# Kernel optimization log

Measured on AMD Instinct MI355X. Metric: run time of the kernel, lower is better.

Reference implementation:

```python
import jax, jax.numpy as jnp
import numpy as np

N, DEG, F = 500000, 16, 128
H1, H2, OUT = 256, 256, 128


def setup_inputs() -> dict:
    key = jax.random.key(0)
    ks = jax.random.split(key, 8)
    s = lambda fan_in: 1.0 / np.sqrt(fan_in)
    return {
        "message": jax.random.normal(ks[0], (N, DEG, F), dtype=jnp.float32),
        "features": jax.random.normal(ks[1], (N, F), dtype=jnp.float32),
        "global_features": jax.random.normal(ks[2], (N, F), dtype=jnp.float32),
        "W1": jax.random.normal(ks[3], (3 * F, H1), dtype=jnp.float32) * s(3 * F),
        "b1": jnp.zeros((H1,), dtype=jnp.float32),
        "W2": jax.random.normal(ks[4], (H1, H2), dtype=jnp.float32) * s(H1),
        "b2": jnp.zeros((H2,), dtype=jnp.float32),
        "W3": jax.random.normal(ks[5], (H2, OUT), dtype=jnp.float32) * s(H2),
        "b3": jnp.zeros((OUT,), dtype=jnp.float32),
    }


def reference(message, features, global_features, W1, b1, W2, b2, W3, b3):
    # mailbox sum-aggregate over neighbors: [N, deg, F] -> [N, F]
    agg = jnp.sum(message, axis=1)
    # concat aggregated messages with node + global features: [N, 3F]
    x = jnp.concatenate([agg, features, global_features], axis=1)
    # MLP: Linear+ReLU, Linear+ReLU, Linear
    h = jax.nn.relu(x @ W1 + b1)
    h = jax.nn.relu(h @ W2 + b2)
    out = h @ W3 + b3
    # row-wise L2 (Frobenius over dim=1) normalization
    norm = jnp.linalg.norm(out, axis=1, keepdims=True)
    return out / (norm + 1e-8)
```

## Files before the change

kernel.cpp:

```cpp
#include <hip/hip_runtime.h>


typedef short short8   __attribute__((ext_vector_type(8)));
typedef short short4_t __attribute__((ext_vector_type(4)));
typedef float f32x4    __attribute__((ext_vector_type(4)));

#define SWZ(row, off) ((off) ^ (((row) & 7) << 4))

__device__ __forceinline__ unsigned short f2bf(float f) {
    unsigned int u = __float_as_uint(f);
    u += 0x7fffu + ((u >> 16) & 1u);
    return (unsigned short)(u >> 16);
}

__global__ void prep_weights(const float* __restrict__ W1,
                             const float* __restrict__ W2,
                             const float* __restrict__ W3,
                             short* __restrict__ pw1,
                             short* __restrict__ pw2,
                             short* __restrict__ pw3) {
    int idx = blockIdx.x * 256 + threadIdx.x;
    if (idx < 98304) {
        int j = idx & 7, l = (idx >> 3) & 63, g = idx >> 9;
        int ks = g % 12, tn = g / 12;
        int n = tn * 16 + (l & 15);
        int k = ks * 32 + ((l >> 4) << 3) + j;
        pw1[idx] = (short)f2bf(W1[k * 256 + n]);
    } else if (idx < 98304 + 65536) {
        int e = idx - 98304;
        int j = e & 7, l = (e >> 3) & 63, g = e >> 9;
        int ks = g & 7, tn = g >> 3;
        int n = tn * 16 + (l & 15);
        int k = ks * 32 + ((l >> 4) << 3) + j;
        pw2[e] = (short)f2bf(W2[k * 256 + n]);
    } else if (idx < 98304 + 65536 + 32768) {
        int e = idx - 98304 - 65536;
        int j = e & 7, l = (e >> 3) & 63, g = e >> 9;
        int ks = g & 7, tn = g >> 3;
        int n = tn * 16 + (l & 15);
        int k = ks * 32 + ((l >> 4) << 3) + j;
        pw3[e] = (short)f2bf(W3[k * 128 + n]);
    }
}

__global__ __launch_bounds__(256) void agg_kernel(
    const float* __restrict__ msg, short* __restrict__ agg, int n_rows)
{
    const int w = threadIdx.x >> 6;
    const int l = threadIdx.x & 63;
    const long long pb = (long long)blockIdx.x * 8 + 2 * w;
    if (pb >= n_rows) return;

    const f32x4* base = (const f32x4*)((const char*)msg + pb * 8192);
    f32x4 tA[8], tB[8];
    const bool okB = (pb + 1) < n_rows;
    #pragma unroll
    for (int i = 0; i < 8; ++i) tA[i] = __builtin_nontemporal_load(base + i * 64 + l);
    if (okB) {
        #pragma unroll
        for (int i = 0; i < 8; ++i) tB[i] = __builtin_nontemporal_load(base + (8 + i) * 64 + l);
    } else {
        #pragma unroll
        for (int i = 0; i < 8; ++i) tB[i] = (f32x4){0.f, 0.f, 0.f, 0.f};
    }
    f32x4 sA = ((tA[0] + tA[1]) + (tA[2] + tA[3])) + ((tA[4] + tA[5]) + (tA[6] + tA[7]));
    f32x4 sB = ((tB[0] + tB[1]) + (tB[2] + tB[3])) + ((tB[4] + tB[5]) + (tB[6] + tB[7]));
    #pragma unroll
    for (int c = 0; c < 4; ++c) {
        sA[c] += __shfl_xor(sA[c], 32);
        sB[c] += __shfl_xor(sB[c], 32);
    }
    f32x4 s = (l < 32) ? sA : sB;
    short4_t s4;
    s4[0] = (short)f2bf(s[0]); s4[1] = (short)f2bf(s[1]);
    s4[2] = (short)f2bf(s[2]); s4[3] = (short)f2bf(s[3]);
    const long long orow = pb + (l >> 5);
    if (orow < n_rows)
        *(short4_t*)(agg + orow * 128 + (l & 31) * 4) = s4;
}

__global__ __launch_bounds__(256, 4) void node_net(
    const short* __restrict__ aggb,
    const float* __restrict__ feat,
    const float* __restrict__ glob,
    const float* __restrict__ b1v,
    const float* __restrict__ b2v,
    const float* __restrict__ b3v,
    const short* __restrict__ pw1,
    const short* __restrict__ pw2,
    const short* __restrict__ pw3,
    float* __restrict__ out,
    int n_rows)
{
    __shared__ char lds[32768];
    char* regA = lds;
    char* regB = lds + 16384;

    const int tid  = threadIdx.x;
    const int lane = tid & 63;
    const int w    = tid >> 6;
    const int lr   = lane & 15;
    const int lk   = lane >> 4;
    const long long r0 = (long long)blockIdx.x * 32;

    const f32x4 zero4 = {0.f, 0.f, 0.f, 0.f};

    f32x4 fr[4], gr[4];
    #pragma unroll
    for (int q = 0; q < 4; ++q) {
        int r = (tid >> 5) + q * 8;
        long long row = r0 + r;
        fr[q] = zero4; gr[q] = zero4;
        if (row < n_rows) {
            fr[q] = __builtin_nontemporal_load((const f32x4*)feat + row * 32 + (tid & 31));
            gr[q] = __builtin_nontemporal_load((const f32x4*)glob + row * 32 + (tid & 31));
        }
    }

    #pragma unroll
    for (int pass = 0; pass < 2; ++pass) {
        int r = tid >> 3;
        int c = (tid & 7) + 8 * pass;
        long long row = r0 + r;
        short8 v = {0, 0, 0, 0, 0, 0, 0, 0};
        if (row < n_rows) v = __builtin_nontemporal_load((const short8*)(aggb + row * 128 + c * 8));
        *(short8*)(regB + SWZ(r, r * 256 + c * 16)) = v;
    }
    __syncthreads();

    #pragma unroll
    for (int q = 0; q < 4; ++q) {
        int r = (tid >> 5) + q * 8;
        short4_t s4;
        s4[0] = (short)f2bf(fr[q][0]); s4[1] = (short)f2bf(fr[q][1]);
        s4[2] = (short)f2bf(fr[q][2]); s4[3] = (short)f2bf(fr[q][3]);
        *(short4_t*)(regA + SWZ(r, r * 256 + (tid & 31) * 8)) = s4;
    }

    f32x4 acc1[2][4];
    #pragma unroll
    for (int ri = 0; ri < 2; ++ri)
        #pragma unroll
        for (int ci = 0; ci < 4; ++ci) acc1[ri][ci] = zero4;

    #pragma unroll
    for (int s = 0; s < 4; ++s) {
        short8 a[2], b[4];
        #pragma unroll
        for (int ri = 0; ri < 2; ++ri) {
            int row = ri * 16 + lr;
            a[ri] = *(const short8*)(regB + SWZ(row, row * 256 + s * 64 + lk * 16));
        }
        #pragma unroll
        for (int ci = 0; ci < 4; ++ci) {
            int tn = w * 4 + ci;
            b[ci] = *(const short8*)(pw1 + (((tn * 12 + s) * 64 + lane) << 3));
        }
        #pragma unroll
        for (int ri = 0; ri < 2; ++ri)
            #pragma unroll
            for (int ci = 0; ci < 4; ++ci)
                acc1[ri][ci] = __builtin_amdgcn_mfma_f32_16x16x32_bf16(
                    a[ri], b[ci], acc1[ri][ci], 0, 0, 0);
    }
    __syncthreads();

    #pragma unroll
    for (int q = 0; q < 4; ++q) {
        int r = (tid >> 5) + q * 8;
        short4_t s4;
        s4[0] = (short)f2bf(gr[q][0]); s4[1] = (short)f2bf(gr[q][1]);
        s4[2] = (short)f2bf(gr[q][2]); s4[3] = (short)f2bf(gr[q][3]);
        *(short4_t*)(regB + 8192 + SWZ(r, r * 256 + (tid & 31) * 8)) = s4;
    }

    #pragma unroll
    for (int s = 0; s < 4; ++s) {
        short8 a[2], b[4];
        #pragma unroll
        for (int ri = 0; ri < 2; ++ri) {
            int row = ri * 16 + lr;
            a[ri] = *(const short8*)(regA + SWZ(row, row * 256 + s * 64 + lk * 16));
        }
        #pragma unroll
        for (int ci = 0; ci < 4; ++ci) {
            int tn = w * 4 + ci;
            b[ci] = *(const short8*)(pw1 + (((tn * 12 + 4 + s) * 64 + lane) << 3));
        }
        #pragma unroll
        for (int ri = 0; ri < 2; ++ri)
            #pragma unroll
            for (int ci = 0; ci < 4; ++ci)
                acc1[ri][ci] = __builtin_amdgcn_mfma_f32_16x16x32_bf16(
                    a[ri], b[ci], acc1[ri][ci], 0, 0, 0);
    }
    __syncthreads();

    #pragma unroll
    for (int s = 0; s < 4; ++s) {
        short8 a[2], b[4];
        #pragma unroll
        for (int ri = 0; ri < 2; ++ri) {
            int row = ri * 16 + lr;
            a[ri] = *(const short8*)(regB + 8192 + SWZ(row, row * 256 + s * 64 + lk * 16));
        }
        #pragma unroll
        for (int ci = 0; ci < 4; ++ci) {
            int tn = w * 4 + ci;
            b[ci] = *(const short8*)(pw1 + (((tn * 12 + 8 + s) * 64 + lane) << 3));
        }
        #pragma unroll
        for (int ri = 0; ri < 2; ++ri)
            #pragma unroll
            for (int ci = 0; ci < 4; ++ci)
                acc1[ri][ci] = __builtin_amdgcn_mfma_f32_16x16x32_bf16(
                    a[ri], b[ci], acc1[ri][ci], 0, 0, 0);
    }

    #pragma unroll
    for (int ci = 0; ci < 4; ++ci) {
        int col = w * 64 + ci * 16 + lr;
        float bias = b1v[col];
        #pragma unroll
        for (int ri = 0; ri < 2; ++ri)
            #pragma unroll
            for (int i = 0; i < 4; ++i) {
                int row = ri * 16 + lk * 4 + i;
                float v = fmaxf(acc1[ri][ci][i] + bias, 0.f);
                *(short*)(regA + SWZ(row, row * 512 + col * 2)) = (short)f2bf(v);
            }
    }
    __syncthreads();

    f32x4 acc2[2][4];
    #pragma unroll
    for (int ri = 0; ri < 2; ++ri)
        #pragma unroll
        for (int ci = 0; ci < 4; ++ci) acc2[ri][ci] = zero4;

    #pragma unroll
    for (int s = 0; s < 8; ++s) {
        short8 a[2], b[4];
        #pragma unroll
        for (int ri = 0; ri < 2; ++ri) {
            int row = ri * 16 + lr;
            a[ri] = *(const short8*)(regA + SWZ(row, row * 512 + s * 64 + lk * 16));
        }
        #pragma unroll
        for (int ci = 0; ci < 4; ++ci) {
            int tn = w * 4 + ci;
            b[ci] = *(const short8*)(pw2 + (((tn * 8 + s) * 64 + lane) << 3));
        }
        #pragma unroll
        for (int ri = 0; ri < 2; ++ri)
            #pragma unroll
            for (int ci = 0; ci < 4; ++ci)
                acc2[ri][ci] = __builtin_amdgcn_mfma_f32_16x16x32_bf16(
                    a[ri], b[ci], acc2[ri][ci], 0, 0, 0);
    }

    #pragma unroll
    for (int ci = 0; ci < 4; ++ci) {
        int col = w * 64 + ci * 16 + lr;
        float bias = b2v[col];
        #pragma unroll
        for (int ri = 0; ri < 2; ++ri)
            #pragma unroll
            for (int i = 0; i < 4; ++i) {
                int row = ri * 16 + lk * 4 + i;
                float v = fmaxf(acc2[ri][ci][i] + bias, 0.f);
                *(short*)(regB + SWZ(row, row * 512 + col * 2)) = (short)f2bf(v);
            }
    }
    __syncthreads();

    f32x4 acc3[2][2];
    #pragma unroll
    for (int ri = 0; ri < 2; ++ri)
        #pragma unroll
        for (int ci = 0; ci < 2; ++ci) acc3[ri][ci] = zero4;

    #pragma unroll
    for (int s = 0; s < 8; ++s) {
        short8 a[2], b[2];
        #pragma unroll
        for (int ri = 0; ri < 2; ++ri) {
            int row = ri * 16 + lr;
            a[ri] = *(const short8*)(regB + SWZ(row, row * 512 + s * 64 + lk * 16));
        }
        #pragma unroll
        for (int ci = 0; ci < 2; ++ci) {
            int tn = w * 2 + ci;
            b[ci] = *(const short8*)(pw3 + (((tn * 8 + s) * 64 + lane) << 3));
        }
        #pragma unroll
        for (int ri = 0; ri < 2; ++ri)
            #pragma unroll
            for (int ci = 0; ci < 2; ++ci)
                acc3[ri][ci] = __builtin_amdgcn_mfma_f32_16x16x32_bf16(
                    a[ri], b[ci], acc3[ri][ci], 0, 0, 0);
    }

    #pragma unroll
    for (int ci = 0; ci < 2; ++ci) {
        int col = w * 32 + ci * 16 + lr;
        float bias = b3v[col];
        #pragma unroll
        for (int ri = 0; ri < 2; ++ri)
            #pragma unroll
            for (int i = 0; i < 4; ++i) {
                int row = ri * 16 + lk * 4 + i;
                float v = acc3[ri][ci][i] + bias;
                *(float*)(regA + SWZ(row, row * 512 + col * 4)) = v;
            }
    }
    __syncthreads();

    #pragma unroll
    for (int pass = 0; pass < 4; ++pass) {
        const int r  = (tid >> 5) + pass * 8;
        const int fl = tid & 31;
        f32x4 v = *(const f32x4*)(regA + SWZ(r, r * 512 + fl * 16));
        float ss = v[0]*v[0] + v[1]*v[1] + v[2]*v[2] + v[3]*v[3];
        ss += __shfl_xor(ss, 1, 32);
        ss += __shfl_xor(ss, 2, 32);
        ss += __shfl_xor(ss, 4, 32);
        ss += __shfl_xor(ss, 8, 32);
        ss += __shfl_xor(ss, 16, 32);
        float inv = 1.f / (sqrtf(ss) + 1e-8f);
        long long row = r0 + r;
        if (row < n_rows) {
            f32x4 o = v * inv;
            __builtin_nontemporal_store(o, (f32x4*)out + row * 32 + fl);
        }
    }
}

extern "C" void kernel_launch(void* const* d_in, const int* in_sizes, int n_in,
                              void* d_out, int out_size, void* d_ws, size_t ws_size,
                              hipStream_t stream) {
    const float* msg  = (const float*)d_in[0];
    const float* feat = (const float*)d_in[1];
    const float* glob = (const float*)d_in[2];
    const float* W1   = (const float*)d_in[3];
    const float* b1   = (const float*)d_in[4];
    const float* W2   = (const float*)d_in[5];
    const float* b2   = (const float*)d_in[6];
    const float* W3   = (const float*)d_in[7];
    const float* b3   = (const float*)d_in[8];
    float* out = (float*)d_out;

    const int n_rows = in_sizes[1] / 128;

    short* pw1  = (short*)d_ws;
    short* pw2  = pw1 + 98304;
    short* pw3  = pw2 + 65536;
    short* aggb = pw3 + 32768;

    hipLaunchKernelGGL(prep_weights, dim3(768), dim3(256), 0, stream,
                       W1, W2, W3, pw1, pw2, pw3);

    const int ablocks = (n_rows + 7) / 8;
    hipLaunchKernelGGL(agg_kernel, dim3(ablocks), dim3(256), 0, stream,
                       msg, aggb, n_rows);

    const int nblocks = (n_rows + 31) / 32;
    hipLaunchKernelGGL(node_net, dim3(nblocks), dim3(256), 0, stream,
                       aggb, feat, glob, b1, b2, b3, pw1, pw2, pw3, out, n_rows);
}
```

Measured before the change: 1.157 ms.

## Fuse neighbor message aggregation into the MLP kernel and drop agg buffer

```diff
diff --git a/kernel.cpp b/kernel.cpp
--- a/kernel.cpp
+++ b/kernel.cpp
@@ -43,44 +43,8 @@
     }
 }
 
-__global__ __launch_bounds__(256) void agg_kernel(
-    const float* __restrict__ msg, short* __restrict__ agg, int n_rows)
-{
-    const int w = threadIdx.x >> 6;
-    const int l = threadIdx.x & 63;
-    const long long pb = (long long)blockIdx.x * 8 + 2 * w;
-    if (pb >= n_rows) return;
-
-    const f32x4* base = (const f32x4*)((const char*)msg + pb * 8192);
-    f32x4 tA[8], tB[8];
-    const bool okB = (pb + 1) < n_rows;
-    #pragma unroll
-    for (int i = 0; i < 8; ++i) tA[i] = __builtin_nontemporal_load(base + i * 64 + l);
-    if (okB) {
-        #pragma unroll
-        for (int i = 0; i < 8; ++i) tB[i] = __builtin_nontemporal_load(base + (8 + i) * 64 + l);
-    } else {
-        #pragma unroll
-        for (int i = 0; i < 8; ++i) tB[i] = (f32x4){0.f, 0.f, 0.f, 0.f};
-    }
-    f32x4 sA = ((tA[0] + tA[1]) + (tA[2] + tA[3])) + ((tA[4] + tA[5]) + (tA[6] + tA[7]));
-    f32x4 sB = ((tB[0] + tB[1]) + (tB[2] + tB[3])) + ((tB[4] + tB[5]) + (tB[6] + tB[7]));
-    #pragma unroll
-    for (int c = 0; c < 4; ++c) {
-        sA[c] += __shfl_xor(sA[c], 32);
-        sB[c] += __shfl_xor(sB[c], 32);
-    }
-    f32x4 s = (l < 32) ? sA : sB;
-    short4_t s4;
-    s4[0] = (short)f2bf(s[0]); s4[1] = (short)f2bf(s[1]);
-    s4[2] = (short)f2bf(s[2]); s4[3] = (short)f2bf(s[3]);
-    const long long orow = pb + (l >> 5);
-    if (orow < n_rows)
-        *(short4_t*)(agg + orow * 128 + (l & 31) * 4) = s4;
-}
-
-__global__ __launch_bounds__(256, 4) void node_net(
-    const short* __restrict__ aggb,
+__global__ __launch_bounds__(256, 4) void node_net_fused(
+    const float* __restrict__ msg,
     const float* __restrict__ feat,
     const float* __restrict__ glob,
     const float* __restrict__ b1v,
@@ -117,14 +81,41 @@
         }
     }
 
-    #pragma unroll
-    for (int pass = 0; pass < 2; ++pass) {
-        int r = tid >> 3;
-        int c = (tid & 7) + 8 * pass;
-        long long row = r0 + r;
-        short8 v = {0, 0, 0, 0, 0, 0, 0, 0};
-        if (row < n_rows) v = __builtin_nontemporal_load((const short8*)(aggb + row * 128 + c * 8));
-        *(short8*)(regB + SWZ(r, r * 256 + c * 16)) = v;
+    #pragma unroll 1
+    for (int pp = 0; pp < 4; ++pp) {
+        const int rA = 8 * w + 2 * pp;
+        const long long rowA = r0 + rA;
+        const f32x4* base = (const f32x4*)msg + rowA * 512;
+        f32x4 tA[8], tB[8];
+        const bool okA = rowA < n_rows;
+        const bool okB = (rowA + 1) < n_rows;
+        if (okA) {
+            #pragma unroll
+            for (int i = 0; i < 8; ++i) tA[i] = __builtin_nontemporal_load(base + i * 64 + lane);
+        } else {
+            #pragma unroll
+            for (int i = 0; i < 8; ++i) tA[i] = zero4;
+        }
+        if (okB) {
+            #pragma unroll
+            for (int i = 0; i < 8; ++i) tB[i] = __builtin_nontemporal_load(base + 512 + i * 64 + lane);
+        } else {
+            #pragma unroll
+            for (int i = 0; i < 8; ++i) tB[i] = zero4;
+        }
+        f32x4 sA = ((tA[0] + tA[1]) + (tA[2] + tA[3])) + ((tA[4] + tA[5]) + (tA[6] + tA[7]));
+        f32x4 sB = ((tB[0] + tB[1]) + (tB[2] + tB[3])) + ((tB[4] + tB[5]) + (tB[6] + tB[7]));
+        #pragma unroll
+        for (int c = 0; c < 4; ++c) {
+            sA[c] += __shfl_xor(sA[c], 32);
+            sB[c] += __shfl_xor(sB[c], 32);
+        }
+        f32x4 s = (lane < 32) ? sA : sB;
+        short4_t s4;
+        s4[0] = (short)f2bf(s[0]); s4[1] = (short)f2bf(s[1]);
+        s4[2] = (short)f2bf(s[2]); s4[3] = (short)f2bf(s[3]);
+        const int orow = rA + (lane >> 5);
+        *(short4_t*)(regB + SWZ(orow, orow * 256 + (lane & 31) * 8)) = s4;
     }
     __syncthreads();
 
@@ -352,19 +343,14 @@
 
     const int n_rows = in_sizes[1] / 128;
 
-    short* pw1  = (short*)d_ws;
-    short* pw2  = pw1 + 98304;
-    short* pw3  = pw2 + 65536;
-    short* aggb = pw3 + 32768;
+    short* pw1 = (short*)d_ws;
+    short* pw2 = pw1 + 98304;
+    short* pw3 = pw2 + 65536;
 
     hipLaunchKernelGGL(prep_weights, dim3(768), dim3(256), 0, stream,
                        W1, W2, W3, pw1, pw2, pw3);
 
-    const int ablocks = (n_rows + 7) / 8;
-    hipLaunchKernelGGL(agg_kernel, dim3(ablocks), dim3(256), 0, stream,
-                       msg, aggb, n_rows);
-
     const int nblocks = (n_rows + 31) / 32;
-    hipLaunchKernelGGL(node_net, dim3(nblocks), dim3(256), 0, stream,
-                       aggb, feat, glob, b1, b2, b3, pw1, pw2, pw3, out, n_rows);
+    hipLaunchKernelGGL(node_net_fused, dim3(nblocks), dim3(256), 0, stream,
+                       msg, feat, glob, b1, b2, b3, pw1, pw2, pw3, out, n_rows);
 }
```

Result: faster. 1.080 ms (-6.7%).
